# Kernel optimization log

Measured on AMD Instinct MI355X. Metric: run time of the kernel, lower is better.

## Reference

```python
import jax, jax.numpy as jnp
import numpy as np

B = 4096
V_ECC, V_ERR = 16, 12
T = 25
C_T = 32            # temporal_out
F_IN = C_T * T      # 800 = ChebConv in_channels
GCN_OUT = 64
HID2 = 256          # hidden_size * 2


def _ring_edge_index(n):
    # undirected ring (both directions), no self loops -- AHA-segment-style adjacency
    s = np.arange(n); t = (s + 1) % n
    return np.stack([np.concatenate([s, t]), np.concatenate([t, s])]).astype(np.int64)


def setup_inputs() -> dict:
    key = jax.random.key(0)
    ks = iter(jax.random.split(key, 24))
    p = lambda shape, sc=0.05: jax.random.normal(next(ks), shape, jnp.float32) * sc
    return {
        "ecc": jax.random.normal(next(ks), (B, V_ECC, T), jnp.float32),
        "err": jax.random.normal(next(ks), (B, V_ERR, T), jnp.float32),
        "conv_ecc_w": p((C_T, 1, 3)), "conv_ecc_b": p((C_T,)),
        "conv_err_w": p((C_T, 1, 3)), "conv_err_b": p((C_T,)),
        "cheb_ecc_W": p((2, F_IN, GCN_OUT)), "cheb_ecc_b": p((GCN_OUT,)),
        "cheb_err_W": p((2, F_IN, GCN_OUT)), "cheb_err_b": p((GCN_OUT,)),
        "ecc_proj_W": p((V_ECC * GCN_OUT, HID2)), "ecc_proj_b": p((HID2,)),
        "err_proj_W": p((V_ERR * GCN_OUT, HID2)), "err_proj_b": p((HID2,)),
        "attn_W": p((HID2, 1)), "attn_b": p((1,)),
        "fc2_W": p((HID2, 1)), "fc2_b": p((1,)),
        "edge_index_ecc": jnp.asarray(_ring_edge_index(V_ECC)),
        "edge_index_err": jnp.asarray(_ring_edge_index(V_ERR)),
    }


def _temporal_conv(x, w, b):
    # torch Conv1d(1, C_T, kernel=3, padding=1) applied per node, then
    # reshape(B, V, C_T*T) exactly like the torch code (channel-major per node).
    Bv, V, T_ = x.shape
    y = jax.lax.conv_general_dilated(x.reshape(Bv * V, 1, T_), w, (1,), [(1, 1)],
                                     dimension_numbers=("NCH", "OIH", "NCH"))
    y = y + b[None, :, None]
    return y.reshape(Bv, V, -1)  # [B, V, C_T*T]


def _cheb_conv(x, edge_index, W, b):
    # PyG ChebConv(K=2, normalization='sym', lambda_max=2.0):
    #   Lhat = 2 L / lambda_max - I = -D^{-1/2} A D^{-1/2}
    #   out  = Tx0 @ W[0] + Tx1 @ W[1] + b,  Tx0 = x, Tx1 = Lhat x
    # Batched over B with a single segment_sum (replaces the per-sample loop).
    src, dst = edge_index[0], edge_index[1]
    V = x.shape[1]
    deg = jax.ops.segment_sum(jnp.ones(src.shape, jnp.float32), src, num_segments=V)
    dis = jnp.where(deg > 0, jax.lax.rsqrt(jnp.maximum(deg, 1.0)), 0.0)
    w_e = -dis[src] * dis[dst]                        # [E]
    msg = x[:, src, :] * w_e[None, :, None]           # [B, E, F] gather
    Tx1 = jax.ops.segment_sum(msg.transpose(1, 0, 2), dst, num_segments=V)  # [V, B, F]
    Tx1 = Tx1.transpose(1, 0, 2)                      # [B, V, F] scatter-add
    return jnp.einsum("bvf,fo->bvo", x, W[0]) + jnp.einsum("bvf,fo->bvo", Tx1, W[1]) + b


def reference(ecc, err, conv_ecc_w, conv_ecc_b, conv_err_w, conv_err_b,
              cheb_ecc_W, cheb_ecc_b, cheb_err_W, cheb_err_b,
              ecc_proj_W, ecc_proj_b, err_proj_W, err_proj_b,
              attn_W, attn_b, fc2_W, fc2_b, edge_index_ecc, edge_index_err):
    Bv = ecc.shape[0]
    ecc_f = _temporal_conv(ecc, conv_ecc_w, conv_ecc_b)   # [B, 16, 800]
    err_f = _temporal_conv(err, conv_err_w, conv_err_b)   # [B, 12, 800]
    ecc_out = _cheb_conv(ecc_f, edge_index_ecc, cheb_ecc_W, cheb_ecc_b)  # [B, 16, 64]
    err_out = _cheb_conv(err_f, edge_index_err, cheb_err_W, cheb_err_b)  # [B, 12, 64]
    # gated fusion
    ecc_g = ecc_out.reshape(Bv, -1) @ ecc_proj_W + ecc_proj_b  # [B, 256]
    err_g = err_out.reshape(Bv, -1) @ err_proj_W + err_proj_b  # [B, 256]
    attn = jax.nn.sigmoid(jnp.tanh(ecc_g + err_g) @ attn_W + attn_b)  # [B, 1]
    fused = attn * ecc_g + (1.0 - attn) * err_g   # latent_layer (gated path skips fc1)
    x = jax.nn.relu(fused) @ fc2_W + fc2_b        # dropout = identity (eval mode)
    return jax.nn.sigmoid(x)                      # [B, 1]
```

## Files before the change

kernel.cpp:

```cpp
#include <hip/hip_runtime.h>
#include <hip/hip_bf16.h>
#include <math.h>


#define TM 16
#define HID2 256
#define KE 400
#define KR 300
#define CE 13
#define CR 10

#define OFF_A0   6400
#define OFF_B0   6656
#define OFF_CV   6912
#define KBF_ECC  7424
#define KBF_ERR  60672

typedef __attribute__((ext_vector_type(8))) short  short8;
typedef __attribute__((ext_vector_type(4))) float  f32x4;

static __device__ __forceinline__ float ldv(const void* p, int i, bool f32) {
    return f32 ? ((const float*)p)[i]
               : __bfloat162float(((const __hip_bfloat16*)p)[i]);
}

static __device__ __forceinline__ bool detect_f32(const void* ecc) {
    unsigned w = ((const unsigned*)ecc)[threadIdx.x & 63];
    int e0 = (w >> 7) & 0xff, e1 = (w >> 23) & 0xff;
    return __any((e0 >= 141) || (e1 >= 141)) != 0;
}

static __device__ __forceinline__ int bswz(int k, int o) {
    int c = k >> 5, q = (k >> 3) & 3, j = k & 7;
    int nt = o >> 4, li = o & 15;
    return (c * 16 + nt) * 512 + (q * 16 + li) * 8 + j;
}

static __device__ __forceinline__ unsigned pack_bf16(float x0, float x1) {
    __hip_bfloat16 h0 = __float2bfloat16(x0), h1 = __float2bfloat16(x1);
    unsigned u0 = *(unsigned short*)&h0, u1 = *(unsigned short*)&h1;
    return (u1 << 16) | u0;
}

__global__ __launch_bounds__(256) void precompute1(
                            const void* __restrict__ ecc,
                            const void* __restrict__ conv_ecc_w,
                            const void* __restrict__ conv_err_w,
                            const void* __restrict__ conv_ecc_b,
                            const void* __restrict__ conv_err_b,
                            const void* __restrict__ cheb_ecc_W,
                            const void* __restrict__ cheb_err_W,
                            float* __restrict__ ws) {
    bool f32 = detect_f32(ecc);
    int tid = threadIdx.x, o = tid & 63, cq = tid >> 6;
    __shared__ float s[256];
    if (blockIdx.x < 100) {
        int m = blockIdx.x / 25, tp = blockIdx.x % 25;
        const void* cw = (m < 2) ? conv_ecc_w : conv_err_w;
        const void* W  = (m < 2) ? cheb_ecc_W : cheb_err_W;
        int wofs = (m & 1) * (800 * 64);
        float acc = 0.f;
        for (int cc = 0; cc < 8; ++cc) {
            int c = cq * 8 + cc;
            #pragma unroll
            for (int k = 0; k < 3; ++k) {
                int t = tp + 1 - k;
                if (t >= 0 && t < 25)
                    acc += ldv(cw, c * 3 + k, f32) * ldv(W, wofs + (c * 25 + t) * 64 + o, f32);
            }
        }
        s[tid] = acc;
        __syncthreads();
        if (tid < 64)
            ws[m * 1600 + tp * 64 + o] = s[tid] + s[tid + 64] + s[tid + 128] + s[tid + 192];
    } else if (blockIdx.x < 108) {
        int q = blockIdx.x - 100;
        int sig = q >> 2, part = q & 3;
        const void* convb = sig ? conv_err_b : conv_ecc_b;
        const void* W     = sig ? cheb_err_W : cheb_ecc_W;
        float p = 0.f;
        #pragma unroll
        for (int cc = 0; cc < 2; ++cc) {
            int c = part * 8 + cq * 2 + cc;
            float bc = ldv(convb, c, f32);
            #pragma unroll 5
            for (int t = 0; t < 25; ++t)
                p += bc * (ldv(W, (c * 25 + t) * 64 + o, f32)
                         - ldv(W, 800 * 64 + (c * 25 + t) * 64 + o, f32));
        }
        s[tid] = p;
        __syncthreads();
        if (tid < 64)
            ws[OFF_CV + (sig * 4 + part) * 64 + o] =
                s[o] + s[o + 64] + s[o + 128] + s[o + 192];
    } else {
        unsigned short* KbE = (unsigned short*)(ws + KBF_ECC);
        unsigned short* KbR = (unsigned short*)(ws + KBF_ERR);
        for (int idx = tid; idx < (16 + 20) * 256; idx += 256) {
            if (idx < 16 * 256) KbE[bswz(400 + (idx >> 8), idx & 255)] = 0;
            else {
                int i2 = idx - 16 * 256;
                KbR[bswz(300 + (i2 >> 8), i2 & 255)] = 0;
            }
        }
    }
}

__global__ __launch_bounds__(256) void precompute2(
                            const void* __restrict__ ecc,
                            const void* __restrict__ ecc_proj_W,
                            const void* __restrict__ err_proj_W,
                            const void* __restrict__ ecc_proj_b,
                            const void* __restrict__ err_proj_b,
                            const void* __restrict__ cheb_ecc_b,
                            const void* __restrict__ cheb_err_b,
                            float* __restrict__ ws) {
    bool f32 = detect_f32(ecc);
    int tid = threadIdx.x, bid = blockIdx.x;
    __shared__ f32x4 wt4[2][64][8];
    __shared__ float red[256];
    __shared__ float cv_s[64];

    if (bid < 112) {
        int sig = bid >= 64;
        int lb  = sig ? bid - 64 : bid;
        int v = lb >> 2, oc = lb & 3;
        int V = sig ? 12 : 16;
        const void* P = sig ? err_proj_W : ecc_proj_W;
        const float* wb0 = ws + (sig ? 3200 : 0);
        const float* wb1 = ws + (sig ? 4800 : 1600);
        float* wf = (float*)wt4;
        f32x4 z = {0.f, 0.f, 0.f, 0.f};
        for (int idx = tid; idx < 2 * 64 * 8; idx += 256)
            ((f32x4*)wt4)[idx] = z;
        __syncthreads();
        for (int idx = tid; idx < 1600; idx += 256) {
            int tp = idx >> 6, j = idx & 63;
            wf[j * 32 + tp]        = wb0[idx];
            wf[2048 + j * 32 + tp] = wb1[idx];
        }
        __syncthreads();

        int ol = tid & 63, tpg = tid >> 6;
        int o = oc * 64 + ol;
        int vp1 = (v + 1) % V, vm1 = (v + V - 1) % V;
        int b0 = v * 64 * HID2 + o, ba = vp1 * 64 * HID2 + o, bb = vm1 * 64 * HID2 + o;
        f32x4 acc0 = z, acc1 = z;
        #pragma unroll 4
        for (int j = 0; j < 64; ++j) {
            float p0 = ldv(P, b0 + j * HID2, f32);
            float pp = ldv(P, ba + j * HID2, f32) + ldv(P, bb + j * HID2, f32);
            float ph = -0.5f * pp;
            f32x4 w0a = wt4[0][j][tpg * 2], w0b = wt4[0][j][tpg * 2 + 1];
            f32x4 w1a = wt4[1][j][tpg * 2], w1b = wt4[1][j][tpg * 2 + 1];
            acc0 += w0a * p0 + w1a * ph;
            acc1 += w0b * p0 + w1b * ph;
        }
        unsigned short* KB = (unsigned short*)(ws + (sig ? KBF_ERR : KBF_ECC));
        #pragma unroll
        for (int i = 0; i < 4; ++i) {
            int tp = tpg * 8 + i;
            if (tp < 25) {
                __hip_bfloat16 h = __float2bfloat16(acc0[i]);
                KB[bswz(v * 25 + tp, o)] = *(unsigned short*)&h;
            }
        }
        #pragma unroll
        for (int i = 0; i < 4; ++i) {
            int tp = tpg * 8 + 4 + i;
            if (tp < 25) {
                __hip_bfloat16 h = __float2bfloat16(acc1[i]);
                KB[bswz(v * 25 + tp, o)] = *(unsigned short*)&h;
            }
        }
    } else {
        int q = bid - 112;
        int sig = q >> 2, oc = q & 3;
        int V = sig ? 12 : 16, nv = V / 4;
        const void* P     = sig ? err_proj_W : ecc_proj_W;
        const void* chebb = sig ? cheb_err_b : cheb_ecc_b;
        const void* pb    = sig ? err_proj_b : ecc_proj_b;
        if (tid < 64) {
            float c = ldv(chebb, tid, f32);
            #pragma unroll
            for (int p2 = 0; p2 < 4; ++p2)
                c += ws[OFF_CV + (sig * 4 + p2) * 64 + tid];
            cv_s[tid] = c;
        }
        __syncthreads();
        int ol = tid & 63, vg = tid >> 6;
        int o = oc * 64 + ol;
        float acc = 0.f;
        for (int vv = 0; vv < nv; ++vv) {
            int v = vg * nv + vv;
            #pragma unroll 4
            for (int j = 0; j < 64; ++j)
                acc += cv_s[j] * ldv(P, (v * 64 + j) * HID2 + o, f32);
        }
        red[tid] = acc;
        __syncthreads();
        if (tid < 64)
            ws[(sig ? OFF_B0 : OFF_A0) + oc * 64 + tid] =
                red[tid] + red[tid + 64] + red[tid + 128] + red[tid + 192]
                + ldv(pb, oc * 64 + tid, f32);
    }
}

#define XR_DW 3328

__global__ __launch_bounds__(512, 2) void main_gemm(
        const void* __restrict__ ecc, const void* __restrict__ err,
        const void* __restrict__ attn_W, const void* __restrict__ attn_b,
        const void* __restrict__ fc2_W, const void* __restrict__ fc2_b,
        const float* __restrict__ ws, void* __restrict__ out) {
    __shared__ float smem[2 * 16 * 257];
    unsigned* xs = (unsigned*)smem;

    bool f32 = detect_f32(ecc);
    int tid  = threadIdx.x;
    int row0 = blockIdx.x * TM;

    for (int idx = tid; idx < 16 * 208; idx += 512) {
        int r = idx / 208, i2 = idx - r * 208;
        unsigned u = 0;
        if (i2 < 200) {
            if (f32) u = pack_bf16(((const float*)ecc)[(row0 + r) * 400 + 2 * i2],
                                   ((const float*)ecc)[(row0 + r) * 400 + 2 * i2 + 1]);
            else     u = ((const unsigned*)ecc)[(row0 + r) * 200 + i2];
        }
        xs[(i2 >> 4) * 256 + r * 16 + (i2 & 15)] = u;
    }
    for (int idx = tid; idx < 16 * 160; idx += 512) {
        int r = idx / 160, i2 = idx - r * 160;
        unsigned u = 0;
        if (i2 < 150) {
            if (f32) u = pack_bf16(((const float*)err)[(row0 + r) * 300 + 2 * i2],
                                   ((const float*)err)[(row0 + r) * 300 + 2 * i2 + 1]);
            else     u = ((const unsigned*)err)[(row0 + r) * 150 + i2];
        }
        xs[XR_DW + (i2 >> 4) * 256 + r * 16 + (i2 & 15)] = u;
    }
    __syncthreads();

    int wv = tid >> 6, lane = tid & 63;
    int m = lane & 15, quad = lane >> 4;
    int nt0 = wv * 2;

    const short8* KbE = (const short8*)(ws + KBF_ECC);
    const short8* KbR = (const short8*)(ws + KBF_ERR);
    const char* abase = (const char*)smem + m * 64 + quad * 16;

    f32x4 acc_e[2] = {{0.f, 0.f, 0.f, 0.f}, {0.f, 0.f, 0.f, 0.f}};
    f32x4 acc_r[2] = {{0.f, 0.f, 0.f, 0.f}, {0.f, 0.f, 0.f, 0.f}};

    #pragma unroll
    for (int c = 0; c < CE; ++c) {
        short8 a = *(const short8*)(abase + c * 1024);
        #pragma unroll
        for (int t = 0; t < 2; ++t)
            acc_e[t] = __builtin_amdgcn_mfma_f32_16x16x32_bf16(
                a, KbE[(c * 16 + nt0 + t) * 64 + lane], acc_e[t], 0, 0, 0);
    }
    #pragma unroll
    for (int c = 0; c < CR; ++c) {
        short8 a = *(const short8*)(abase + XR_DW * 4 + c * 1024);
        #pragma unroll
        for (int t = 0; t < 2; ++t)
            acc_r[t] = __builtin_amdgcn_mfma_f32_16x16x32_bf16(
                a, KbR[(c * 16 + nt0 + t) * 64 + lane], acc_r[t], 0, 0, 0);
    }
    __syncthreads();

    float* ge_s = smem;
    float* gr_s = smem + 16 * 257;
    #pragma unroll
    for (int t = 0; t < 2; ++t) {
        int col = (nt0 + t) * 16 + m;
        float a0v = ws[OFF_A0 + col], b0v = ws[OFF_B0 + col];
        #pragma unroll
        for (int i = 0; i < 4; ++i) {
            int row = quad * 4 + i;
            ge_s[row * 257 + col] = acc_e[t][i] + a0v;
            gr_s[row * 257 + col] = acc_r[t][i] + b0v;
        }
    }
    __syncthreads();

    float aw[4], fw[4];
    #pragma unroll
    for (int j = 0; j < 4; ++j) {
        aw[j] = ldv(attn_W, lane + 64 * j, f32);
        fw[j] = ldv(fc2_W,  lane + 64 * j, f32);
    }
    float ab = ldv(attn_b, 0, f32), fb = ldv(fc2_b, 0, f32);
    #pragma unroll
    for (int rr = 0; rr < 2; ++rr) {
        int r = wv * 2 + rr;
        float ge[4], gr[4];
        #pragma unroll
        for (int j = 0; j < 4; ++j) {
            ge[j] = ge_s[r * 257 + lane + 64 * j];
            gr[j] = gr_s[r * 257 + lane + 64 * j];
        }
        float p = 0.f;
        #pragma unroll
        for (int j = 0; j < 4; ++j) p += tanhf(ge[j] + gr[j]) * aw[j];
        #pragma unroll
        for (int off = 32; off; off >>= 1) p += __shfl_down(p, off);
        float a = 1.f / (1.f + expf(-(__shfl(p, 0) + ab)));
        float p2 = 0.f;
        #pragma unroll
        for (int j = 0; j < 4; ++j) {
            float fu = a * ge[j] + (1.f - a) * gr[j];
            p2 += fmaxf(fu, 0.f) * fw[j];
        }
        #pragma unroll
        for (int off = 32; off; off >>= 1) p2 += __shfl_down(p2, off);
        if (lane == 0) {
            float vout = 1.f / (1.f + expf(-(p2 + fb)));
            if (f32) ((float*)out)[row0 + r] = vout;
            else     ((__hip_bfloat16*)out)[row0 + r] = __float2bfloat16(vout);
        }
    }
}

extern "C" void kernel_launch(void* const* d_in, const int* in_sizes, int n_in,
                              void* d_out, int out_size, void* d_ws, size_t ws_size,
                              hipStream_t stream) {
    const void* ecc        = d_in[0];
    const void* err        = d_in[1];
    const void* conv_ecc_w = d_in[2];
    const void* conv_ecc_b = d_in[3];
    const void* conv_err_w = d_in[4];
    const void* conv_err_b = d_in[5];
    const void* cheb_ecc_W = d_in[6];
    const void* cheb_ecc_b = d_in[7];
    const void* cheb_err_W = d_in[8];
    const void* cheb_err_b = d_in[9];
    const void* ecc_proj_W = d_in[10];
    const void* ecc_proj_b = d_in[11];
    const void* err_proj_W = d_in[12];
    const void* err_proj_b = d_in[13];
    const void* attn_W     = d_in[14];
    const void* attn_b     = d_in[15];
    const void* fc2_W      = d_in[16];
    const void* fc2_b      = d_in[17];
    float* ws = (float*)d_ws;

    precompute1<<<109, 256, 0, stream>>>(ecc, conv_ecc_w, conv_err_w, conv_ecc_b,
                                         conv_err_b, cheb_ecc_W, cheb_err_W, ws);
    precompute2<<<120, 256, 0, stream>>>(ecc, ecc_proj_W, err_proj_W, ecc_proj_b,
                                         err_proj_b, cheb_ecc_b, cheb_err_b, ws);
    main_gemm<<<4096 / TM, 512, 0, stream>>>(ecc, err, attn_W, attn_b, fc2_W, fc2_b,
                                             ws, d_out);
}
```

Measured before the change: 139.1 us.

## Fuse precompute and main GEMM into one cooperative kernel with grid syncs

Merges the two weight-precompute kernels and the main MFMA GEMM into a single cooperative launch of 256 blocks. Two grid-wide barriers separate the stages, and each block stages its input rows into LDS before the first barrier so that load overlaps the precompute work. The goal is to remove two kernel launches and their inter-kernel gaps. The cost is grid.sync overhead and a single-wave occupancy bound (launch_bounds 512,1). The old three-kernel path remains as a fallback if the cooperative launch fails, and some loop unroll factors are raised.

```diff
diff --git a/kernel.cpp b/kernel.cpp
--- a/kernel.cpp
+++ b/kernel.cpp
@@ -1,12 +1,13 @@
 #include <hip/hip_runtime.h>
 #include <hip/hip_bf16.h>
+#include <hip/hip_cooperative_groups.h>
 #include <math.h>
+
+namespace cg = cooperative_groups;
 
 
 #define TM 16
 #define HID2 256
-#define KE 400
-#define KR 300
 #define CE 13
 #define CR 10
 
@@ -15,6 +16,7 @@
 #define OFF_CV   6912
 #define KBF_ECC  7424
 #define KBF_ERR  60672
+#define XR_DW    3328
 
 typedef __attribute__((ext_vector_type(8))) short  short8;
 typedef __attribute__((ext_vector_type(4))) float  f32x4;
@@ -40,6 +42,284 @@
     __hip_bfloat16 h0 = __float2bfloat16(x0), h1 = __float2bfloat16(x1);
     unsigned u0 = *(unsigned short*)&h0, u1 = *(unsigned short*)&h1;
     return (u1 << 16) | u0;
+}
+
+__global__ __launch_bounds__(512, 1) void fused(
+        const void* __restrict__ ecc, const void* __restrict__ err,
+        const void* __restrict__ conv_ecc_w, const void* __restrict__ conv_ecc_b,
+        const void* __restrict__ conv_err_w, const void* __restrict__ conv_err_b,
+        const void* __restrict__ cheb_ecc_W, const void* __restrict__ cheb_ecc_b,
+        const void* __restrict__ cheb_err_W, const void* __restrict__ cheb_err_b,
+        const void* __restrict__ ecc_proj_W, const void* __restrict__ ecc_proj_b,
+        const void* __restrict__ err_proj_W, const void* __restrict__ err_proj_b,
+        const void* __restrict__ attn_W, const void* __restrict__ attn_b,
+        const void* __restrict__ fc2_W, const void* __restrict__ fc2_b,
+        float* __restrict__ ws, void* __restrict__ out) {
+    __shared__ float smem[2 * 16 * 257];
+    __shared__ f32x4 wt4[2][64][8];
+    __shared__ float red[512];
+    __shared__ float cv_s[64];
+    unsigned* xs = (unsigned*)smem;
+
+    bool f32 = detect_f32(ecc);
+    int tid = threadIdx.x, bid = blockIdx.x;
+    int row0 = bid * TM;
+    cg::grid_group grid = cg::this_grid();
+
+    for (int idx = tid; idx < 16 * 208; idx += 512) {
+        int r = idx / 208, i2 = idx - r * 208;
+        unsigned u = 0;
+        if (i2 < 200) {
+            if (f32) u = pack_bf16(((const float*)ecc)[(row0 + r) * 400 + 2 * i2],
+                                   ((const float*)ecc)[(row0 + r) * 400 + 2 * i2 + 1]);
+            else     u = ((const unsigned*)ecc)[(row0 + r) * 200 + i2];
+        }
+        xs[(i2 >> 4) * 256 + r * 16 + (i2 & 15)] = u;
+    }
+    for (int idx = tid; idx < 16 * 160; idx += 512) {
+        int r = idx / 160, i2 = idx - r * 160;
+        unsigned u = 0;
+        if (i2 < 150) {
+            if (f32) u = pack_bf16(((const float*)err)[(row0 + r) * 300 + 2 * i2],
+                                   ((const float*)err)[(row0 + r) * 300 + 2 * i2 + 1]);
+            else     u = ((const unsigned*)err)[(row0 + r) * 150 + i2];
+        }
+        xs[XR_DW + (i2 >> 4) * 256 + r * 16 + (i2 & 15)] = u;
+    }
+
+    if (bid < 100) {
+        int m = bid / 25, tp = bid % 25;
+        const void* cw = (m < 2) ? conv_ecc_w : conv_err_w;
+        const void* W  = (m < 2) ? cheb_ecc_W : cheb_err_W;
+        int wofs = (m & 1) * (800 * 64);
+        int o = tid & 63, cq = tid >> 6;
+        float acc = 0.f;
+        #pragma unroll
+        for (int cc = 0; cc < 4; ++cc) {
+            int c = cq * 4 + cc;
+            #pragma unroll
+            for (int k = 0; k < 3; ++k) {
+                int t = tp + 1 - k;
+                if (t >= 0 && t < 25)
+                    acc += ldv(cw, c * 3 + k, f32) * ldv(W, wofs + (c * 25 + t) * 64 + o, f32);
+            }
+        }
+        red[tid] = acc;
+        __syncthreads();
+        if (tid < 64) {
+            float s = 0.f;
+            #pragma unroll
+            for (int g = 0; g < 8; ++g) s += red[tid + 64 * g];
+            ws[m * 1600 + tp * 64 + tid] = s;
+        }
+    } else if (bid < 108) {
+        int q = bid - 100, sig = q >> 2, part = q & 3;
+        const void* convb = sig ? conv_err_b : conv_ecc_b;
+        const void* W     = sig ? cheb_err_W : cheb_ecc_W;
+        int o = tid & 63, cq = tid >> 6;
+        int c = part * 8 + cq;
+        float bc = ldv(convb, c, f32);
+        float p = 0.f;
+        #pragma unroll 5
+        for (int t = 0; t < 25; ++t)
+            p += ldv(W, (c * 25 + t) * 64 + o, f32)
+               - ldv(W, 51200 + (c * 25 + t) * 64 + o, f32);
+        red[tid] = bc * p;
+        __syncthreads();
+        if (tid < 64) {
+            float s = 0.f;
+            #pragma unroll
+            for (int g = 0; g < 8; ++g) s += red[tid + 64 * g];
+            ws[OFF_CV + (sig * 4 + part) * 64 + tid] = s;
+        }
+    } else if (bid == 108) {
+        unsigned short* KbE = (unsigned short*)(ws + KBF_ECC);
+        unsigned short* KbR = (unsigned short*)(ws + KBF_ERR);
+        for (int idx = tid; idx < 36 * 256; idx += 512) {
+            if (idx < 16 * 256) KbE[bswz(400 + (idx >> 8), idx & 255)] = 0;
+            else {
+                int i2 = idx - 16 * 256;
+                KbR[bswz(300 + (i2 >> 8), i2 & 255)] = 0;
+            }
+        }
+    }
+
+    __threadfence();
+    grid.sync();
+
+    if (bid < 56) {
+        int u0 = bid * 2;
+        int sig = (u0 >= 64);
+        int lb0 = u0 - (sig ? 64 : 0);
+        int v = lb0 >> 2;
+        int V = sig ? 12 : 16;
+        const void* P = sig ? err_proj_W : ecc_proj_W;
+        const float* wb0 = ws + (sig ? 3200 : 0);
+        const float* wb1 = ws + (sig ? 4800 : 1600);
+        float* wf = (float*)wt4;
+        f32x4 z = {0.f, 0.f, 0.f, 0.f};
+        for (int idx = tid; idx < 1024; idx += 512)
+            ((f32x4*)wt4)[idx] = z;
+        __syncthreads();
+        for (int idx = tid; idx < 1600; idx += 512) {
+            int tp = idx >> 6, j = idx & 63;
+            wf[j * 32 + tp]        = wb0[idx];
+            wf[2048 + j * 32 + tp] = wb1[idx];
+        }
+        __syncthreads();
+
+        int hid = tid & 255, ol = hid & 63, tpg = hid >> 6;
+        int oc = (lb0 & 3) + (tid >> 8);
+        int o = oc * 64 + ol;
+        int vp1 = (v + 1) % V, vm1 = (v + V - 1) % V;
+        int b0 = v * 64 * HID2 + o, ba = vp1 * 64 * HID2 + o, bb = vm1 * 64 * HID2 + o;
+        f32x4 acc0 = z, acc1 = z;
+        #pragma unroll 8
+        for (int j = 0; j < 64; ++j) {
+            float p0 = ldv(P, b0 + j * HID2, f32);
+            float pp = ldv(P, ba + j * HID2, f32) + ldv(P, bb + j * HID2, f32);
+            float ph = -0.5f * pp;
+            f32x4 w0a = wt4[0][j][tpg * 2], w0b = wt4[0][j][tpg * 2 + 1];
+            f32x4 w1a = wt4[1][j][tpg * 2], w1b = wt4[1][j][tpg * 2 + 1];
+            acc0 += w0a * p0 + w1a * ph;
+            acc1 += w0b * p0 + w1b * ph;
+        }
+        unsigned short* KB = (unsigned short*)(ws + (sig ? KBF_ERR : KBF_ECC));
+        #pragma unroll
+        for (int i = 0; i < 4; ++i) {
+            int tp = tpg * 8 + i;
+            if (tp < 25) {
+                __hip_bfloat16 h = __float2bfloat16(acc0[i]);
+                KB[bswz(v * 25 + tp, o)] = *(unsigned short*)&h;
+            }
+        }
+        #pragma unroll
+        for (int i = 0; i < 4; ++i) {
+            int tp = tpg * 8 + 4 + i;
+            if (tp < 25) {
+                __hip_bfloat16 h = __float2bfloat16(acc1[i]);
+                KB[bswz(v * 25 + tp, o)] = *(unsigned short*)&h;
+            }
+        }
+    } else if (bid < 64) {
+        int q = bid - 56, sig = q >> 2, oc = q & 3;
+        int V = sig ? 12 : 16;
+        const void* P     = sig ? err_proj_W : ecc_proj_W;
+        const void* chebb = sig ? cheb_err_b : cheb_ecc_b;
+        const void* pb    = sig ? err_proj_b : ecc_proj_b;
+        if (tid < 64) {
+            float c = ldv(chebb, tid, f32);
+            #pragma unroll
+            for (int pp = 0; pp < 4; ++pp)
+                c += ws[OFF_CV + (sig * 4 + pp) * 64 + tid];
+            cv_s[tid] = c;
+        }
+        __syncthreads();
+        int ol = tid & 63, Jg = tid >> 6;
+        int o = oc * 64 + ol;
+        int JL = (V * 64) >> 3;
+        int Jb = Jg * JL;
+        float acc = 0.f;
+        #pragma unroll 8
+        for (int jj = 0; jj < JL; ++jj) {
+            int J = Jb + jj;
+            acc += cv_s[J & 63] * ldv(P, J * HID2 + o, f32);
+        }
+        red[tid] = acc;
+        __syncthreads();
+        if (tid < 64) {
+            float s = ldv(pb, oc * 64 + tid, f32);
+            #pragma unroll
+            for (int g = 0; g < 8; ++g) s += red[tid + 64 * g];
+            ws[(sig ? OFF_B0 : OFF_A0) + oc * 64 + tid] = s;
+        }
+    }
+
+    __threadfence();
+    grid.sync();
+
+    {
+        int wv = tid >> 6, lane = tid & 63;
+        int m = lane & 15, quad = lane >> 4;
+        int nt0 = wv * 2;
+
+        const short8* KbE = (const short8*)(ws + KBF_ECC);
+        const short8* KbR = (const short8*)(ws + KBF_ERR);
+        const char* abase = (const char*)smem + m * 64 + quad * 16;
+
+        f32x4 acc_e[2] = {{0.f, 0.f, 0.f, 0.f}, {0.f, 0.f, 0.f, 0.f}};
+        f32x4 acc_r[2] = {{0.f, 0.f, 0.f, 0.f}, {0.f, 0.f, 0.f, 0.f}};
+
+        #pragma unroll
+        for (int c = 0; c < CE; ++c) {
+            short8 a = *(const short8*)(abase + c * 1024);
+            #pragma unroll
+            for (int t = 0; t < 2; ++t)
+                acc_e[t] = __builtin_amdgcn_mfma_f32_16x16x32_bf16(
+                    a, KbE[(c * 16 + nt0 + t) * 64 + lane], acc_e[t], 0, 0, 0);
+        }
+        #pragma unroll
+        for (int c = 0; c < CR; ++c) {
+            short8 a = *(const short8*)(abase + XR_DW * 4 + c * 1024);
+            #pragma unroll
+            for (int t = 0; t < 2; ++t)
+                acc_r[t] = __builtin_amdgcn_mfma_f32_16x16x32_bf16(
+                    a, KbR[(c * 16 + nt0 + t) * 64 + lane], acc_r[t], 0, 0, 0);
+        }
+        __syncthreads();
+
+        float* ge_s = smem;
+        float* gr_s = smem + 16 * 257;
+        #pragma unroll
+        for (int t = 0; t < 2; ++t) {
+            int col = (nt0 + t) * 16 + m;
+            float a0v = ws[OFF_A0 + col], b0v = ws[OFF_B0 + col];
+            #pragma unroll
+            for (int i = 0; i < 4; ++i) {
+                int row = quad * 4 + i;
+                ge_s[row * 257 + col] = acc_e[t][i] + a0v;
+                gr_s[row * 257 + col] = acc_r[t][i] + b0v;
+            }
+        }
+        __syncthreads();
+
+        float aw[4], fw[4];
+        #pragma unroll
+        for (int j = 0; j < 4; ++j) {
+            aw[j] = ldv(attn_W, lane + 64 * j, f32);
+            fw[j] = ldv(fc2_W,  lane + 64 * j, f32);
+        }
+        float ab = ldv(attn_b, 0, f32), fb = ldv(fc2_b, 0, f32);
+        #pragma unroll
+        for (int rr = 0; rr < 2; ++rr) {
+            int r = wv * 2 + rr;
+            float ge[4], gr[4];
+            #pragma unroll
+            for (int j = 0; j < 4; ++j) {
+                ge[j] = ge_s[r * 257 + lane + 64 * j];
+                gr[j] = gr_s[r * 257 + lane + 64 * j];
+            }
+            float p = 0.f;
+            #pragma unroll
+            for (int j = 0; j < 4; ++j) p += tanhf(ge[j] + gr[j]) * aw[j];
+            #pragma unroll
+            for (int off = 32; off; off >>= 1) p += __shfl_down(p, off);
+            float a = 1.f / (1.f + expf(-(__shfl(p, 0) + ab)));
+            float p2 = 0.f;
+            #pragma unroll
+            for (int j = 0; j < 4; ++j) {
+                float fu = a * ge[j] + (1.f - a) * gr[j];
+                p2 += fmaxf(fu, 0.f) * fw[j];
+            }
+            #pragma unroll
+            for (int off = 32; off; off >>= 1) p2 += __shfl_down(p2, off);
+            if (lane == 0) {
+                float vout = 1.f / (1.f + expf(-(p2 + fb)));
+                if (f32) ((float*)out)[row0 + r] = vout;
+                else     ((__hip_bfloat16*)out)[row0 + r] = __float2bfloat16(vout);
+            }
+        }
+    }
 }
 
 __global__ __launch_bounds__(256) void precompute1(
@@ -146,7 +426,7 @@
         int vp1 = (v + 1) % V, vm1 = (v + V - 1) % V;
         int b0 = v * 64 * HID2 + o, ba = vp1 * 64 * HID2 + o, bb = vm1 * 64 * HID2 + o;
         f32x4 acc0 = z, acc1 = z;
-        #pragma unroll 4
+        #pragma unroll 8
         for (int j = 0; j < 64; ++j) {
             float p0 = ldv(P, b0 + j * HID2, f32);
             float pp = ldv(P, ba + j * HID2, f32) + ldv(P, bb + j * HID2, f32);
@@ -193,7 +473,7 @@
         float acc = 0.f;
         for (int vv = 0; vv < nv; ++vv) {
             int v = vg * nv + vv;
-            #pragma unroll 4
+            #pragma unroll 8
             for (int j = 0; j < 64; ++j)
                 acc += cv_s[j] * ldv(P, (v * 64 + j) * HID2 + o, f32);
         }
@@ -205,8 +485,6 @@
                 + ldv(pb, oc * 64 + tid, f32);
     }
 }
-
-#define XR_DW 3328
 
 __global__ __launch_bounds__(512, 2) void main_gemm(
         const void* __restrict__ ecc, const void* __restrict__ err,
@@ -346,11 +624,29 @@
     const void* fc2_W      = d_in[16];
     const void* fc2_b      = d_in[17];
     float* ws = (float*)d_ws;
-
-    precompute1<<<109, 256, 0, stream>>>(ecc, conv_ecc_w, conv_err_w, conv_ecc_b,
-                                         conv_err_b, cheb_ecc_W, cheb_err_W, ws);
-    precompute2<<<120, 256, 0, stream>>>(ecc, ecc_proj_W, err_proj_W, ecc_proj_b,
-                                         err_proj_b, cheb_ecc_b, cheb_err_b, ws);
-    main_gemm<<<4096 / TM, 512, 0, stream>>>(ecc, err, attn_W, attn_b, fc2_W, fc2_b,
-                                             ws, d_out);
-}
+    void* outp = d_out;
+
+    void* args[] = {
+        (void*)&ecc, (void*)&err,
+        (void*)&conv_ecc_w, (void*)&conv_ecc_b,
+        (void*)&conv_err_w, (void*)&conv_err_b,
+        (void*)&cheb_ecc_W, (void*)&cheb_ecc_b,
+        (void*)&cheb_err_W, (void*)&cheb_err_b,
+        (void*)&ecc_proj_W, (void*)&ecc_proj_b,
+        (void*)&err_proj_W, (void*)&err_proj_b,
+        (void*)&attn_W, (void*)&attn_b,
+        (void*)&fc2_W, (void*)&fc2_b,
+        (void*)&ws, (void*)&outp
+    };
+    hipError_t e = hipLaunchCooperativeKernel(fused, dim3(256), dim3(512),
+                                              args, 0, stream);
+    if (e != hipSuccess) {
+        (void)hipGetLastError();
+        precompute1<<<109, 256, 0, stream>>>(ecc, conv_ecc_w, conv_err_w, conv_ecc_b,
+                                             conv_err_b, cheb_ecc_W, cheb_err_W, ws);
+        precompute2<<<120, 256, 0, stream>>>(ecc, ecc_proj_W, err_proj_W, ecc_proj_b,
+                                             err_proj_b, cheb_ecc_b, cheb_err_b, ws);
+        main_gemm<<<4096 / TM, 512, 0, stream>>>(ecc, err, attn_W, attn_b, fc2_W,
+                                                 fc2_b, ws, d_out);
+    }
+}
```

New measurement: 295.5 us. 112% more time.
